# Performance work log

Measured on AMD Instinct MI355X. Metric: run time of the kernel, lower is better.

The kernel has to match this reference:

```python
import jax, jax.numpy as jnp
import numpy as np

N = 50000
E = 800000
IN_DIM = 256
HID_DIM = 256
OUT_DIM = 128


def _gcn(x, src, dst, W, b):
    # PyG GCNConv: h = W x; add self-loops; sym-normalized scatter-add; + bias
    h = x @ W  # [N, out]
    deg = jax.ops.segment_sum(jnp.ones_like(dst, dtype=h.dtype), dst, num_segments=N)
    dinv = jax.lax.rsqrt(jnp.maximum(deg, 1e-12))
    norm = dinv[src] * dinv[dst]  # [E+N]
    msg = h[src] * norm[:, None]  # gather + scale
    out = jax.ops.segment_sum(msg, dst, num_segments=N)  # scatter-add
    return out + b


def _with_self_loops(edge):
    loops = jnp.arange(N, dtype=edge.dtype)
    src = jnp.concatenate([edge[0], loops])
    dst = jnp.concatenate([edge[1], loops])
    return src, dst


def setup_inputs() -> dict:
    key = jax.random.key(0)
    ks = jax.random.split(key, 20)
    d = {}
    d['x'] = jax.random.normal(ks[0], (N, IN_DIM), dtype=jnp.float32)
    d['edge_ppi'] = jax.random.randint(ks[1], (2, E), 0, N, dtype=jnp.int32)
    d['edge_path'] = jax.random.randint(ks[2], (2, E), 0, N, dtype=jnp.int32)
    d['edge_go'] = jax.random.randint(ks[3], (2, E), 0, N, dtype=jnp.int32)
    i = 4
    for name in ['ppi', 'path', 'go']:
        s1 = 1.0 / np.sqrt(IN_DIM)
        s2 = 1.0 / np.sqrt(HID_DIM)
        d[f'{name}_w1'] = jax.random.uniform(ks[i], (IN_DIM, HID_DIM), jnp.float32, -s1, s1); i += 1
        d[f'{name}_b1'] = jnp.zeros((HID_DIM,), jnp.float32)
        d[f'{name}_w2'] = jax.random.uniform(ks[i], (HID_DIM, OUT_DIM), jnp.float32, -s2, s2); i += 1
        d[f'{name}_b2'] = jnp.zeros((OUT_DIM,), jnp.float32)
    sa = 1.0 / np.sqrt(OUT_DIM)
    d['attn_w'] = jax.random.uniform(ks[i], (OUT_DIM, 1), jnp.float32, -sa, sa)
    d['attn_b'] = jnp.zeros((1,), jnp.float32)
    return d


def reference(x, edge_ppi, edge_path, edge_go,
              ppi_w1, ppi_b1, ppi_w2, ppi_b2,
              path_w1, path_b1, path_w2, path_b2,
              go_w1, go_b1, go_w2, go_b2,
              attn_w, attn_b):
    feats = []
    for edge, w1, b1, w2, b2 in [
        (edge_ppi, ppi_w1, ppi_b1, ppi_w2, ppi_b2),
        (edge_path, path_w1, path_b1, path_w2, path_b2),
        (edge_go, go_w1, go_b1, go_w2, go_b2),
    ]:
        src, dst = _with_self_loops(edge)
        h = jax.nn.relu(_gcn(x, src, dst, w1, b1))
        feats.append(_gcn(h, src, dst, w2, b2))
    all_feat = jnp.stack(feats, axis=1)  # [N, 3, out]
    attn = jax.nn.softmax(all_feat @ attn_w + attn_b, axis=1)  # [N, 3, 1]
    return jnp.sum(all_feat * attn, axis=1)  # [N, out]
```

## Files before the change

kernel.cpp:

```cpp
#include <hip/hip_runtime.h>

#define NN 50000
#define NE 800000
#define BINS 98
#define CAP 12288
#define EPB 4096
#define P1B ((NE + EPB - 1) / EPB)
#define BINB (3 * P1B)
#define WB ((NN + 3) / 4)

typedef __attribute__((ext_vector_type(8))) short short8;
typedef __attribute__((ext_vector_type(4))) float f32x4;
typedef __attribute__((ext_vector_type(8))) unsigned short ushort8v;
typedef __attribute__((ext_vector_type(4))) unsigned short ushort4v;
typedef _Float16 half8 __attribute__((ext_vector_type(8)));

__device__ __forceinline__ ushort f2h(float f) {
    _Float16 h = (_Float16)f;
    return __builtin_bit_cast(ushort, h);
}
__device__ __forceinline__ float h2f(ushort u) {
    return (float)__builtin_bit_cast(_Float16, u);
}

__device__ __forceinline__ int wave_incl_scan(int v, int lane) {
#pragma unroll
    for (int d = 1; d < 64; d <<= 1) {
        int u = __shfl_up(v, d);
        if (lane >= d) v += u;
    }
    return v;
}


__global__ __launch_bounds__(256) void k_setup(
    const int* __restrict__ e0, const int* __restrict__ e1,
    const int* __restrict__ e2, int* __restrict__ g_cur,
    unsigned* __restrict__ g_bins,
    const float* __restrict__ x, ushort* __restrict__ x16,
    const float* __restrict__ w1a, const float* __restrict__ w1b,
    const float* __restrict__ w1c, ushort* __restrict__ BT1all,
    const float* __restrict__ w2a, const float* __restrict__ w2b,
    const float* __restrict__ w2c, ushort* __restrict__ BT2all) {
    const int tid = threadIdx.x;

    if (blockIdx.x < BINB) {
        const int br = blockIdx.x / P1B;
        const int cb = blockIdx.x % P1B;
        const int* ep = (br == 0 ? e0 : br == 1 ? e1 : e2);
        const int e_base = cb * EPB;

        __shared__ int s_cnt[BINS];
        __shared__ int s_start[BINS];
        __shared__ int s_cur[BINS];
        __shared__ int s_gb[BINS];
        __shared__ unsigned s_stage[EPB];

        if (tid < BINS) s_cnt[tid] = 0;
        __syncthreads();

        int4 s4[4], d4[4];
        bool valid[4];
#pragma unroll
        for (int i = 0; i < 4; ++i) {
            int idx = e_base + i * 1024 + tid * 4;
            valid[i] = (idx < NE);
            if (valid[i]) {
                s4[i] = *(const int4*)&ep[idx];
                d4[i] = *(const int4*)&ep[NE + idx];
                atomicAdd(&s_cnt[d4[i].x >> 9], 1);
                atomicAdd(&s_cnt[d4[i].y >> 9], 1);
                atomicAdd(&s_cnt[d4[i].z >> 9], 1);
                atomicAdd(&s_cnt[d4[i].w >> 9], 1);
            }
        }
        __syncthreads();
        if (tid == 0) {
            int run = 0;
            for (int b = 0; b < BINS; ++b) {
                s_start[b] = run;
                run += s_cnt[b];
            }
        }
        __syncthreads();
        if (tid < BINS) {
            s_cur[tid] = s_start[tid];
            int c = s_cnt[tid];
            int pc = (c + 15) & ~15;
            s_gb[tid] = (c > 0) ? atomicAdd(&g_cur[br * BINS + tid], pc) : 0;
        }
        __syncthreads();

#pragma unroll
        for (int i = 0; i < 4; ++i) {
            if (valid[i]) {
                int ss[4] = {s4[i].x, s4[i].y, s4[i].z, s4[i].w};
                int dd[4] = {d4[i].x, d4[i].y, d4[i].z, d4[i].w};
#pragma unroll
                for (int q = 0; q < 4; ++q) {
                    int bin = dd[q] >> 9;
                    int pos = atomicAdd(&s_cur[bin], 1);
                    s_stage[pos] = ((unsigned)(dd[q] & 511) << 16) | (unsigned)ss[q];
                }
            }
        }
        __syncthreads();

        for (int b = 0; b < BINS; ++b) {
            int c = s_cnt[b];
            if (c == 0) continue;
            int st = s_start[b];
            int gb = s_gb[b];
            int pc = (c + 15) & ~15;
            if (gb + pc > CAP) pc = (gb < CAP) ? (CAP - gb) : 0;
            size_t obase = (size_t)(br * BINS + b) * CAP + gb;
            for (int j = tid; j < pc; j += 256)
                g_bins[obase + j] = (j < c) ? s_stage[st + j] : 0x80000000u;
        }
        return;
    }

    int bb = blockIdx.x - BINB;
    if (bb < WB) {
        const int wid = tid >> 6, lane = tid & 63;
        const int row = bb * 4 + wid;
        if (row >= NN) return;
        float4 v = *(const float4*)&x[(size_t)row * 256 + lane * 4];
        ushort4 o;
        o.x = f2h(v.x); o.y = f2h(v.y); o.z = f2h(v.z); o.w = f2h(v.w);
        *(ushort4*)&x16[(size_t)row * 256 + lane * 4] = o;
        return;
    }
    bb -= WB;
    if (bb < 768) {
        int idx = bb * 256 + tid;
        int b = idx >> 16, r = idx & 65535;
        int k = r >> 8, n = r & 255;
        const float* W = (b == 0 ? w1a : b == 1 ? w1b : w1c);
        BT1all[(size_t)b * 65536 + (size_t)n * 256 + k] = f2h(W[r]);
        return;
    }
    bb -= 768;
    {
        int idx = bb * 256 + tid;
        int b = idx >> 15, r = idx & 32767;
        int k = r >> 7, n = r & 127;
        const float* W = (b == 0 ? w2a : b == 1 ? w2b : w2c);
        BT2all[(size_t)b * 32768 + (size_t)n * 256 + k] = f2h(W[r]);
    }
}


#define BGB 391

__global__ __launch_bounds__(512) void k_build_gemm1(
    const unsigned* __restrict__ g_bins, const int* __restrict__ g_cur,
    ushort* __restrict__ g_csr, int* __restrict__ seg3, int* __restrict__ cnt3,
    float* __restrict__ dinv3,
    const ushort* __restrict__ x16, const ushort* __restrict__ BT1all,
    ushort* __restrict__ hs16all) {
    __shared__ ushort sA[2][128 * 32];
    __shared__ ushort sB[2][256 * 32];
    __shared__ int s_cnt[512];
    __shared__ int s_wsum[8];

    const int t = threadIdx.x, lane = t & 63, wid = t >> 6;

    if (blockIdx.x < 3 * BINS) {
        const int bid = blockIdx.x;
        const int br = bid / BINS;
        const int b2 = bid % BINS;
        const size_t base = (size_t)bid * CAP;
        const int node0 = b2 << 9;

        s_cnt[t] = 0;
        __syncthreads();

        const int total = min(g_cur[bid], CAP);
        for (int j = t; j < total; j += 512) {
            unsigned p = g_bins[base + j];
            if (!(p & 0x80000000u)) atomicAdd(&s_cnt[(p >> 16) & 0x1FF], 1);
        }
        __syncthreads();

        int c = s_cnt[t];
        int incl = wave_incl_scan(c, lane);
        if (lane == 63) s_wsum[wid] = incl;
        __syncthreads();
        int wpre = 0;
        for (int i = 0; i < wid; ++i) wpre += s_wsum[i];
        int ex = wpre + incl - c;

        int node = node0 + t;
        if (node < NN) {
            int g = br * NN + node;
            seg3[g] = (int)base + ex;
            cnt3[g] = c;
            dinv3[g] = rsqrtf((float)(c + 1));
        }
        __syncthreads();
        s_cnt[t] = ex;
        __syncthreads();

        for (int j = t; j < total; j += 512) {
            unsigned p = g_bins[base + j];
            if (!(p & 0x80000000u)) {
                int loc = (p >> 16) & 0x1FF;
                int pos = atomicAdd(&s_cnt[loc], 1);
                g_csr[base + pos] = (ushort)(p & 0xFFFFu);
            }
        }
        return;
    }

    constexpr int BM = 128, BN = 256, N = 256, KK = 256, BK = 32;
    constexpr int NW = 8, WGN = 4, NSTEP = KK / BK;
    const int sbid = blockIdx.x - 3 * BINS;
    int q = sbid >> 3, r = sbid & 7;
    int bid = (q / 3) * 8 + r;
    int kb = q % 3;
    if (bid >= BGB) return;

    const ushort* BT = BT1all + (size_t)kb * 65536;
    ushort* C = hs16all + (size_t)kb * NN * 256;
    const int wm = (wid / WGN) * 64, wn = (wid % WGN) * 64;
    const int bm = bid * BM;

    f32x4 zero = {0.f, 0.f, 0.f, 0.f};
    f32x4 acc[4][4];
#pragma unroll
    for (int m = 0; m < 4; ++m)
#pragma unroll
        for (int n = 0; n < 4; ++n) acc[m][n] = zero;

    auto stage = [&](int buf, int kt) {
        {
            int off = wid << 10;
            int la = off + lane * 16;
            int row = la >> 6;
            int slot = (la >> 4) & 3;
            int scol = (slot ^ (row & 3)) << 4;
            int grow = bm + row;
            if (grow > NN - 1) grow = NN - 1;
            const char* ga = (const char*)x16 + (size_t)grow * (KK * 2) + kt * 2 + scol;
            __builtin_amdgcn_global_load_lds(
                (__attribute__((address_space(1))) const void*)ga,
                (__attribute__((address_space(3))) void*)((char*)sA[buf] + off), 16, 0, 0);
        }
#pragma unroll
        for (int i = 0; i < 2; ++i) {
            int off = (wid + i * NW) << 10;
            int la = off + lane * 16;
            int row = la >> 6;
            int slot = (la >> 4) & 3;
            int scol = (slot ^ (row & 3)) << 4;
            const char* ga = (const char*)BT + (size_t)row * (KK * 2) + kt * 2 + scol;
            __builtin_amdgcn_global_load_lds(
                (__attribute__((address_space(1))) const void*)ga,
                (__attribute__((address_space(3))) void*)((char*)sB[buf] + off), 16, 0, 0);
        }
    };

    stage(0, 0);
    __syncthreads();

    int cur = 0;
    for (int ts = 0; ts < NSTEP; ++ts) {
        if (ts + 1 < NSTEP) stage(cur ^ 1, (ts + 1) * BK);

        const int s = lane >> 4;
        const int r0 = lane & 15;
        short8 af[4], bf[4];
#pragma unroll
        for (int m = 0; m < 4; ++m) {
            int row = wm + m * 16 + r0;
            af[m] = *(const short8*)((const char*)sA[cur] + row * 64 + ((s ^ (row & 3)) << 4));
        }
#pragma unroll
        for (int n = 0; n < 4; ++n) {
            int row = wn + n * 16 + r0;
            bf[n] = *(const short8*)((const char*)sB[cur] + row * 64 + ((s ^ (row & 3)) << 4));
        }
#pragma unroll
        for (int m = 0; m < 4; ++m)
#pragma unroll
            for (int n = 0; n < 4; ++n)
                acc[m][n] = __builtin_amdgcn_mfma_f32_16x16x32_f16(
                    __builtin_bit_cast(half8, af[m]), __builtin_bit_cast(half8, bf[n]),
                    acc[m][n], 0, 0, 0);
        __syncthreads();
        cur ^= 1;
    }

    const int cr0 = (lane >> 4) * 4;
    const int cc = lane & 15;
#pragma unroll
    for (int m = 0; m < 4; ++m) {
#pragma unroll
        for (int rg = 0; rg < 4; ++rg) {
            int row = bm + wm + m * 16 + cr0 + rg;
            if (row < NN) {
#pragma unroll
                for (int n = 0; n < 4; ++n)
                    C[(size_t)row * N + wn + n * 16 + cc] = f2h(acc[m][n][rg]);
            }
        }
    }
}


__global__ __launch_bounds__(256) void k_gemm2(
    const ushort* __restrict__ h1all, const ushort* __restrict__ BT2all,
    const float* __restrict__ dinv3, ushort* __restrict__ hs2all) {
    constexpr int BM = 128, BN = 128, N = 128, KK = 256, BK = 32;
    constexpr int NW = 4, WGN = 2, NSTEP = KK / BK;
    constexpr int MT = (NN + BM - 1) / BM;
    __shared__ ushort sA[2][BM * 32];
    __shared__ ushort sB[2][BN * 32];
    const int kb = blockIdx.x / MT;
    const int bid = blockIdx.x % MT;
    const ushort* Ab = h1all + (size_t)kb * NN * 256;
    const ushort* BT = BT2all + (size_t)kb * 32768;
    const float* dinv = dinv3 + (size_t)kb * NN;
    ushort* C = hs2all + (size_t)kb * NN * 128;
    const int t = threadIdx.x, lane = t & 63, wid = t >> 6;
    const int wm = (wid / WGN) * 64, wn = (wid % WGN) * 64;
    const int bm = bid * BM;

    f32x4 zero = {0.f, 0.f, 0.f, 0.f};
    f32x4 acc[4][4];
#pragma unroll
    for (int m = 0; m < 4; ++m)
#pragma unroll
        for (int n = 0; n < 4; ++n) acc[m][n] = zero;

    auto stage = [&](int buf, int kt) {
#pragma unroll
        for (int i = 0; i < 2; ++i) {
            int off = (wid + i * NW) << 10;
            int la = off + lane * 16;
            int row = la >> 6;
            int slot = (la >> 4) & 3;
            int scol = (slot ^ (row & 3)) << 4;
            int grow = bm + row;
            if (grow > NN - 1) grow = NN - 1;
            const char* ga = (const char*)Ab + (size_t)grow * (KK * 2) + kt * 2 + scol;
            __builtin_amdgcn_global_load_lds(
                (__attribute__((address_space(1))) const void*)ga,
                (__attribute__((address_space(3))) void*)((char*)sA[buf] + off), 16, 0, 0);
        }
#pragma unroll
        for (int i = 0; i < 2; ++i) {
            int off = (wid + i * NW) << 10;
            int la = off + lane * 16;
            int row = la >> 6;
            int slot = (la >> 4) & 3;
            int scol = (slot ^ (row & 3)) << 4;
            const char* ga = (const char*)BT + (size_t)row * (KK * 2) + kt * 2 + scol;
            __builtin_amdgcn_global_load_lds(
                (__attribute__((address_space(1))) const void*)ga,
                (__attribute__((address_space(3))) void*)((char*)sB[buf] + off), 16, 0, 0);
        }
    };

    stage(0, 0);
    __syncthreads();

    int cur = 0;
    for (int ts = 0; ts < NSTEP; ++ts) {
        if (ts + 1 < NSTEP) stage(cur ^ 1, (ts + 1) * BK);

        const int s = lane >> 4;
        const int r0 = lane & 15;
        short8 af[4], bf[4];
#pragma unroll
        for (int m = 0; m < 4; ++m) {
            int row = wm + m * 16 + r0;
            af[m] = *(const short8*)((const char*)sA[cur] + row * 64 + ((s ^ (row & 3)) << 4));
        }
#pragma unroll
        for (int n = 0; n < 4; ++n) {
            int row = wn + n * 16 + r0;
            bf[n] = *(const short8*)((const char*)sB[cur] + row * 64 + ((s ^ (row & 3)) << 4));
        }
#pragma unroll
        for (int m = 0; m < 4; ++m)
#pragma unroll
            for (int n = 0; n < 4; ++n)
                acc[m][n] = __builtin_amdgcn_mfma_f32_16x16x32_f16(
                    __builtin_bit_cast(half8, af[m]), __builtin_bit_cast(half8, bf[n]),
                    acc[m][n], 0, 0, 0);
        __syncthreads();
        cur ^= 1;
    }

    const int cr0 = (lane >> 4) * 4;
    const int cc = lane & 15;
#pragma unroll
    for (int m = 0; m < 4; ++m) {
#pragma unroll
        for (int rg = 0; rg < 4; ++rg) {
            int row = bm + wm + m * 16 + cr0 + rg;
            if (row < NN) {
                float dv = dinv[row];
#pragma unroll
                for (int n = 0; n < 4; ++n)
                    C[(size_t)row * N + wn + n * 16 + cc] = f2h(acc[m][n][rg] * dv);
            }
        }
    }
}


#define UTOT (3 * 12500)

__global__ __launch_bounds__(256) void k_agg1(const ushort* __restrict__ hs16all,
                                              const int* __restrict__ seg3,
                                              const int* __restrict__ cnt3,
                                              const ushort* __restrict__ g_csr,
                                              const float* __restrict__ dinv3,
                                              const float* __restrict__ b1a,
                                              const float* __restrict__ b1b,
                                              const float* __restrict__ b1c,
                                              ushort* __restrict__ h1all) {
    const int x = blockIdx.x & 7, j = blockIdx.x >> 3;
    const int start = (x * UTOT) >> 3;
    const int end = ((x + 1) * UTOT) >> 3;
    const int u = start + j;
    if (u >= end) return;
    const int b = u / 12500;
    const int blk = u % 12500;

    const int wid = threadIdx.x >> 6;
    const int lane = threadIdx.x & 63;
    const int node = blk * 4 + wid;
    if (node >= NN) return;
    const int half = lane >> 5, l32 = lane & 31;
    const int g = b * NN + node;
    const ushort* hs = hs16all + (size_t)b * NN * 256;
    const float* dv = dinv3 + (size_t)b * NN;
    const ushort* csr = g_csr + seg3[g];
    const int len = cnt3[g] + 1;
    const size_t colb = (size_t)l32 * 8;

    float acc[8] = {0.f, 0.f, 0.f, 0.f, 0.f, 0.f, 0.f, 0.f};
    int i = half;
    for (; i + 6 < len; i += 8) {
        int s0 = (i == 0) ? node : (int)csr[i - 1];
        int s1 = (int)csr[i + 1];
        int s2 = (int)csr[i + 3];
        int s3 = (int)csr[i + 5];
        float d0 = dv[s0], d1 = dv[s1], d2 = dv[s2], d3 = dv[s3];
        ushort8v v0 = *(const ushort8v*)&hs[(size_t)s0 * 256 + colb];
        ushort8v v1 = *(const ushort8v*)&hs[(size_t)s1 * 256 + colb];
        ushort8v v2 = *(const ushort8v*)&hs[(size_t)s2 * 256 + colb];
        ushort8v v3 = *(const ushort8v*)&hs[(size_t)s3 * 256 + colb];
#pragma unroll
        for (int jq = 0; jq < 8; ++jq)
            acc[jq] += (d0 * h2f(v0[jq]) + d1 * h2f(v1[jq])) +
                       (d2 * h2f(v2[jq]) + d3 * h2f(v3[jq]));
    }
    for (; i < len; i += 2) {
        int s = (i == 0) ? node : (int)csr[i - 1];
        float d = dv[s];
        ushort8v v = *(const ushort8v*)&hs[(size_t)s * 256 + colb];
#pragma unroll
        for (int jq = 0; jq < 8; ++jq) acc[jq] += d * h2f(v[jq]);
    }
#pragma unroll
    for (int jq = 0; jq < 8; ++jq) acc[jq] += __shfl_xor(acc[jq], 32);

    if (half == 0) {
        const float* bias = (b == 0 ? b1a : b == 1 ? b1b : b1c);
        const float di = dv[node];
        ushort8v o;
#pragma unroll
        for (int jq = 0; jq < 8; ++jq) {
            float r = fmaxf(di * acc[jq] + bias[l32 * 8 + jq], 0.f);
            o[jq] = f2h(r);
        }
        *(ushort8v*)&h1all[((size_t)b * NN + node) * 256 + colb] = o;
    }
}


__global__ __launch_bounds__(256) void k_final(const ushort* __restrict__ hs2all,
                                               const int* __restrict__ seg3,
                                               const int* __restrict__ cnt3,
                                               const ushort* __restrict__ g_csr,
                                               const float* __restrict__ dinv3,
                                               const float* __restrict__ b2a,
                                               const float* __restrict__ b2b,
                                               const float* __restrict__ b2c,
                                               const float* __restrict__ attn_w,
                                               const float* __restrict__ attn_b,
                                               float* __restrict__ out) {
    const int wid = threadIdx.x >> 6;
    const int lane = threadIdx.x & 63;
    const int node = blockIdx.x * 4 + wid;
    if (node >= NN) return;
    const int half = lane >> 5, l32 = lane & 31;
    const size_t colb = (size_t)l32 * 4;

    float f[3][4];
#pragma unroll
    for (int b = 0; b < 3; ++b) {
        const int g = b * NN + node;
        const ushort* hs = hs2all + (size_t)b * NN * 128;
        const ushort* csr = g_csr + seg3[g];
        const int len = cnt3[g] + 1;
        float acc[4] = {0.f, 0.f, 0.f, 0.f};
        int i = half;
        for (; i + 6 < len; i += 8) {
            int s0 = (i == 0) ? node : (int)csr[i - 1];
            int s1 = (int)csr[i + 1];
            int s2 = (int)csr[i + 3];
            int s3 = (int)csr[i + 5];
            ushort4v v0 = *(const ushort4v*)&hs[(size_t)s0 * 128 + colb];
            ushort4v v1 = *(const ushort4v*)&hs[(size_t)s1 * 128 + colb];
            ushort4v v2 = *(const ushort4v*)&hs[(size_t)s2 * 128 + colb];
            ushort4v v3 = *(const ushort4v*)&hs[(size_t)s3 * 128 + colb];
#pragma unroll
            for (int j = 0; j < 4; ++j)
                acc[j] += (h2f(v0[j]) + h2f(v1[j])) + (h2f(v2[j]) + h2f(v3[j]));
        }
        for (; i < len; i += 2) {
            int s = (i == 0) ? node : (int)csr[i - 1];
            ushort4v v = *(const ushort4v*)&hs[(size_t)s * 128 + colb];
#pragma unroll
            for (int j = 0; j < 4; ++j) acc[j] += h2f(v[j]);
        }
#pragma unroll
        for (int j = 0; j < 4; ++j) acc[j] += __shfl_xor(acc[j], 32);
        const float* bias = (b == 0 ? b2a : b == 1 ? b2b : b2c);
        const float di = dinv3[g];
#pragma unroll
        for (int j = 0; j < 4; ++j) f[b][j] = di * acc[j] + bias[l32 * 4 + j];
    }

    float4 w = *(const float4*)&attn_w[l32 * 4];
    float s0 = f[0][0] * w.x + f[0][1] * w.y + f[0][2] * w.z + f[0][3] * w.w;
    float s1 = f[1][0] * w.x + f[1][1] * w.y + f[1][2] * w.z + f[1][3] * w.w;
    float s2 = f[2][0] * w.x + f[2][1] * w.y + f[2][2] * w.z + f[2][3] * w.w;
#pragma unroll
    for (int m = 16; m >= 1; m >>= 1) {
        s0 += __shfl_xor(s0, m);
        s1 += __shfl_xor(s1, m);
        s2 += __shfl_xor(s2, m);
    }
    float bb = attn_b[0];
    s0 += bb; s1 += bb; s2 += bb;
    float mx = fmaxf(s0, fmaxf(s1, s2));
    float e0 = expf(s0 - mx), e1 = expf(s1 - mx), e2 = expf(s2 - mx);
    float inv = 1.f / (e0 + e1 + e2);
    e0 *= inv; e1 *= inv; e2 *= inv;

    if (half == 0) {
        float4 o;
        o.x = f[0][0] * e0 + f[1][0] * e1 + f[2][0] * e2;
        o.y = f[0][1] * e0 + f[1][1] * e1 + f[2][1] * e2;
        o.z = f[0][2] * e0 + f[1][2] * e1 + f[2][2] * e2;
        o.w = f[0][3] * e0 + f[1][3] * e1 + f[2][3] * e2;
        *(float4*)&out[(size_t)node * 128 + colb] = o;
    }
}


extern "C" void kernel_launch(void* const* d_in, const int* in_sizes, int n_in,
                              void* d_out, int out_size, void* d_ws, size_t ws_size,
                              hipStream_t stream) {
    const float* x = (const float*)d_in[0];
    const int* e0 = (const int*)d_in[1];
    const int* e1 = (const int*)d_in[2];
    const int* e2 = (const int*)d_in[3];
    const float* attn_w = (const float*)d_in[16];
    const float* attn_b = (const float*)d_in[17];

    char* ws = (char*)d_ws;
    size_t off = 0;
    auto alloc = [&](size_t bytes) -> void* {
        void* p = ws + off;
        off += (bytes + 255) & ~(size_t)255;
        return p;
    };

    int* g_cur      = (int*)alloc(3 * BINS * 4);
    int* seg3       = (int*)alloc((size_t)3 * NN * 4);
    int* cnt3       = (int*)alloc((size_t)3 * NN * 4);
    float* dinv3    = (float*)alloc((size_t)3 * NN * 4);
    ushort* g_csr   = (ushort*)alloc((size_t)3 * BINS * CAP * 2);
    ushort* x16     = (ushort*)alloc((size_t)NN * 256 * 2);
    ushort* hs16all = (ushort*)alloc((size_t)3 * NN * 256 * 2);
    ushort* h1all   = (ushort*)alloc((size_t)3 * NN * 256 * 2);
    unsigned* g_bins = (unsigned*)h1all;
    ushort* hs2all  = (ushort*)alloc((size_t)3 * NN * 128 * 2);
    ushort* BT1all  = (ushort*)alloc((size_t)3 * 256 * 256 * 2);
    ushort* BT2all  = (ushort*)alloc((size_t)3 * 128 * 256 * 2);

    hipMemsetAsync(g_cur, 0, 3 * BINS * 4, stream);

    k_setup<<<BINB + WB + 768 + 384, 256, 0, stream>>>(
        e0, e1, e2, g_cur, g_bins, x, x16,
        (const float*)d_in[4], (const float*)d_in[8], (const float*)d_in[12], BT1all,
        (const float*)d_in[6], (const float*)d_in[10], (const float*)d_in[14], BT2all);

    k_build_gemm1<<<3 * BINS + 1176, 512, 0, stream>>>(
        g_bins, g_cur, g_csr, seg3, cnt3, dinv3, x16, BT1all, hs16all);

    k_agg1<<<8 * ((UTOT + 7) / 8), 256, 0, stream>>>(
        hs16all, seg3, cnt3, g_csr, dinv3,
        (const float*)d_in[5], (const float*)d_in[9], (const float*)d_in[13], h1all);

    k_gemm2<<<3 * 391, 256, 0, stream>>>(h1all, BT2all, dinv3, hs2all);

    k_final<<<WB, 256, 0, stream>>>(hs2all, seg3, cnt3, g_csr, dinv3,
                                    (const float*)d_in[7], (const float*)d_in[11],
                                    (const float*)d_in[15], attn_w, attn_b,
                                    (float*)d_out);
}
```

Measured before the change: 403.1 us.

## Fuse layer-1 aggregation with layer-2 GEMM via shared-memory tile

Merges the first-layer neighbor aggregation and the second-layer GEMM into one kernel. Each block aggregates 64 nodes into a swizzled LDS tile, then runs MFMA against W2 read straight from global memory. This drops the h1 round trip through HBM and one kernel launch. In exchange, g_bins now needs its own buffer, each block serializes 16 nodes per wave, there is less parallelism (2346 blocks of 64 nodes instead of 37500 blocks of 4 nodes), and B fragments are no longer staged through LDS.

```diff
diff --git a/kernel.cpp b/kernel.cpp
--- a/kernel.cpp
+++ b/kernel.cpp
@@ -213,7 +213,7 @@
         return;
     }
 
-    constexpr int BM = 128, BN = 256, N = 256, KK = 256, BK = 32;
+    constexpr int BM = 128, N = 256, KK = 256, BK = 32;
     constexpr int NW = 8, WGN = 4, NSTEP = KK / BK;
     const int sbid = blockIdx.x - 3 * BINS;
     int q = sbid >> 3, r = sbid & 7;
@@ -309,177 +309,113 @@
 }
 
 
-__global__ __launch_bounds__(256) void k_gemm2(
-    const ushort* __restrict__ h1all, const ushort* __restrict__ BT2all,
-    const float* __restrict__ dinv3, ushort* __restrict__ hs2all) {
-    constexpr int BM = 128, BN = 128, N = 128, KK = 256, BK = 32;
-    constexpr int NW = 4, WGN = 2, NSTEP = KK / BK;
-    constexpr int MT = (NN + BM - 1) / BM;
-    __shared__ ushort sA[2][BM * 32];
-    __shared__ ushort sB[2][BN * 32];
-    const int kb = blockIdx.x / MT;
-    const int bid = blockIdx.x % MT;
-    const ushort* Ab = h1all + (size_t)kb * NN * 256;
-    const ushort* BT = BT2all + (size_t)kb * 32768;
-    const float* dinv = dinv3 + (size_t)kb * NN;
-    ushort* C = hs2all + (size_t)kb * NN * 128;
+__global__ __launch_bounds__(256) void k_agg1g2(
+    const ushort* __restrict__ hs16all, const int* __restrict__ seg3,
+    const int* __restrict__ cnt3, const ushort* __restrict__ g_csr,
+    const float* __restrict__ dinv3,
+    const float* __restrict__ b1a, const float* __restrict__ b1b,
+    const float* __restrict__ b1c,
+    const ushort* __restrict__ BT2all, ushort* __restrict__ hs2all) {
+    constexpr int TPB = (NN + 63) / 64;
+    const int br = blockIdx.x / TPB;
+    const int blk = blockIdx.x % TPB;
+    const int node0 = blk * 64;
     const int t = threadIdx.x, lane = t & 63, wid = t >> 6;
-    const int wm = (wid / WGN) * 64, wn = (wid % WGN) * 64;
-    const int bm = bid * BM;
-
+    const int half = lane >> 5, l32 = lane & 31;
+
+    __shared__ ushort h1s[64 * 256];
+
+    const ushort* hs = hs16all + (size_t)br * NN * 256;
+    const float* dv = dinv3 + (size_t)br * NN;
+    const float* bias = (br == 0 ? b1a : br == 1 ? b1b : b1c);
+    const size_t colb = (size_t)l32 * 8;
+
+#pragma unroll 1
+    for (int q = 0; q < 16; ++q) {
+        const int r = wid * 16 + q;
+        const int node = node0 + r;
+        if (node < NN) {
+            const int g = br * NN + node;
+            const ushort* csr = g_csr + seg3[g];
+            const int len = cnt3[g] + 1;
+
+            float acc[8] = {0.f, 0.f, 0.f, 0.f, 0.f, 0.f, 0.f, 0.f};
+            int i = half;
+            for (; i + 6 < len; i += 8) {
+                int s0 = (i == 0) ? node : (int)csr[i - 1];
+                int s1 = (int)csr[i + 1];
+                int s2 = (int)csr[i + 3];
+                int s3 = (int)csr[i + 5];
+                float d0 = dv[s0], d1 = dv[s1], d2 = dv[s2], d3 = dv[s3];
+                ushort8v v0 = *(const ushort8v*)&hs[(size_t)s0 * 256 + colb];
+                ushort8v v1 = *(const ushort8v*)&hs[(size_t)s1 * 256 + colb];
+                ushort8v v2 = *(const ushort8v*)&hs[(size_t)s2 * 256 + colb];
+                ushort8v v3 = *(const ushort8v*)&hs[(size_t)s3 * 256 + colb];
+#pragma unroll
+                for (int j = 0; j < 8; ++j)
+                    acc[j] += (d0 * h2f(v0[j]) + d1 * h2f(v1[j])) +
+                              (d2 * h2f(v2[j]) + d3 * h2f(v3[j]));
+            }
+            for (; i < len; i += 2) {
+                int s = (i == 0) ? node : (int)csr[i - 1];
+                float d = dv[s];
+                ushort8v v = *(const ushort8v*)&hs[(size_t)s * 256 + colb];
+#pragma unroll
+                for (int j = 0; j < 8; ++j) acc[j] += d * h2f(v[j]);
+            }
+#pragma unroll
+            for (int j = 0; j < 8; ++j) acc[j] += __shfl_xor(acc[j], 32);
+
+            if (half == 0) {
+                const float di = dv[node];
+                ushort8v o;
+#pragma unroll
+                for (int j = 0; j < 8; ++j) {
+                    float rr = fmaxf(di * acc[j] + bias[l32 * 8 + j], 0.f);
+                    o[j] = f2h(rr);
+                }
+                *(ushort8v*)((char*)h1s + r * 512 + ((l32 ^ (r & 7)) << 4)) = o;
+            }
+        } else if (half == 0) {
+            ushort8v z = {0, 0, 0, 0, 0, 0, 0, 0};
+            *(ushort8v*)((char*)h1s + r * 512 + ((l32 ^ (r & 7)) << 4)) = z;
+        }
+    }
+    __syncthreads();
+
+    const ushort* BT2 = BT2all + (size_t)br * 32768;
+    const int r0 = lane & 15, s = lane >> 4;
     f32x4 zero = {0.f, 0.f, 0.f, 0.f};
-    f32x4 acc[4][4];
-#pragma unroll
-    for (int m = 0; m < 4; ++m)
-#pragma unroll
-        for (int n = 0; n < 4; ++n) acc[m][n] = zero;
-
-    auto stage = [&](int buf, int kt) {
-#pragma unroll
-        for (int i = 0; i < 2; ++i) {
-            int off = (wid + i * NW) << 10;
-            int la = off + lane * 16;
-            int row = la >> 6;
-            int slot = (la >> 4) & 3;
-            int scol = (slot ^ (row & 3)) << 4;
-            int grow = bm + row;
-            if (grow > NN - 1) grow = NN - 1;
-            const char* ga = (const char*)Ab + (size_t)grow * (KK * 2) + kt * 2 + scol;
-            __builtin_amdgcn_global_load_lds(
-                (__attribute__((address_space(1))) const void*)ga,
-                (__attribute__((address_space(3))) void*)((char*)sA[buf] + off), 16, 0, 0);
-        }
-#pragma unroll
-        for (int i = 0; i < 2; ++i) {
-            int off = (wid + i * NW) << 10;
-            int la = off + lane * 16;
-            int row = la >> 6;
-            int slot = (la >> 4) & 3;
-            int scol = (slot ^ (row & 3)) << 4;
-            const char* ga = (const char*)BT + (size_t)row * (KK * 2) + kt * 2 + scol;
-            __builtin_amdgcn_global_load_lds(
-                (__attribute__((address_space(1))) const void*)ga,
-                (__attribute__((address_space(3))) void*)((char*)sB[buf] + off), 16, 0, 0);
-        }
-    };
-
-    stage(0, 0);
-    __syncthreads();
-
-    int cur = 0;
-    for (int ts = 0; ts < NSTEP; ++ts) {
-        if (ts + 1 < NSTEP) stage(cur ^ 1, (ts + 1) * BK);
-
-        const int s = lane >> 4;
-        const int r0 = lane & 15;
-        short8 af[4], bf[4];
-#pragma unroll
-        for (int m = 0; m < 4; ++m) {
-            int row = wm + m * 16 + r0;
-            af[m] = *(const short8*)((const char*)sA[cur] + row * 64 + ((s ^ (row & 3)) << 4));
-        }
-#pragma unroll
-        for (int n = 0; n < 4; ++n) {
-            int row = wn + n * 16 + r0;
-            bf[n] = *(const short8*)((const char*)sB[cur] + row * 64 + ((s ^ (row & 3)) << 4));
-        }
-#pragma unroll
-        for (int m = 0; m < 4; ++m)
-#pragma unroll
-            for (int n = 0; n < 4; ++n)
-                acc[m][n] = __builtin_amdgcn_mfma_f32_16x16x32_f16(
-                    __builtin_bit_cast(half8, af[m]), __builtin_bit_cast(half8, bf[n]),
-                    acc[m][n], 0, 0, 0);
-        __syncthreads();
-        cur ^= 1;
-    }
-
+    f32x4 acc2[8];
+#pragma unroll
+    for (int n = 0; n < 8; ++n) acc2[n] = zero;
+    const int arow = wid * 16 + r0;
+#pragma unroll
+    for (int ks = 0; ks < 8; ++ks) {
+        const int kt = ks * 32;
+        const int slot = (ks * 4 + s) ^ (r0 & 7);
+        short8 a = *(const short8*)((const char*)h1s + arow * 512 + (slot << 4));
+#pragma unroll
+        for (int n = 0; n < 8; ++n) {
+            short8 bfr = *(const short8*)&BT2[(size_t)(n * 16 + r0) * 256 + kt + s * 8];
+            acc2[n] = __builtin_amdgcn_mfma_f32_16x16x32_f16(
+                __builtin_bit_cast(half8, a), __builtin_bit_cast(half8, bfr),
+                acc2[n], 0, 0, 0);
+        }
+    }
+
+    const int cc = lane & 15;
     const int cr0 = (lane >> 4) * 4;
-    const int cc = lane & 15;
-#pragma unroll
-    for (int m = 0; m < 4; ++m) {
-#pragma unroll
-        for (int rg = 0; rg < 4; ++rg) {
-            int row = bm + wm + m * 16 + cr0 + rg;
-            if (row < NN) {
-                float dv = dinv[row];
-#pragma unroll
-                for (int n = 0; n < 4; ++n)
-                    C[(size_t)row * N + wn + n * 16 + cc] = f2h(acc[m][n][rg] * dv);
-            }
-        }
-    }
-}
-
-
-#define UTOT (3 * 12500)
-
-__global__ __launch_bounds__(256) void k_agg1(const ushort* __restrict__ hs16all,
-                                              const int* __restrict__ seg3,
-                                              const int* __restrict__ cnt3,
-                                              const ushort* __restrict__ g_csr,
-                                              const float* __restrict__ dinv3,
-                                              const float* __restrict__ b1a,
-                                              const float* __restrict__ b1b,
-                                              const float* __restrict__ b1c,
-                                              ushort* __restrict__ h1all) {
-    const int x = blockIdx.x & 7, j = blockIdx.x >> 3;
-    const int start = (x * UTOT) >> 3;
-    const int end = ((x + 1) * UTOT) >> 3;
-    const int u = start + j;
-    if (u >= end) return;
-    const int b = u / 12500;
-    const int blk = u % 12500;
-
-    const int wid = threadIdx.x >> 6;
-    const int lane = threadIdx.x & 63;
-    const int node = blk * 4 + wid;
-    if (node >= NN) return;
-    const int half = lane >> 5, l32 = lane & 31;
-    const int g = b * NN + node;
-    const ushort* hs = hs16all + (size_t)b * NN * 256;
-    const float* dv = dinv3 + (size_t)b * NN;
-    const ushort* csr = g_csr + seg3[g];
-    const int len = cnt3[g] + 1;
-    const size_t colb = (size_t)l32 * 8;
-
-    float acc[8] = {0.f, 0.f, 0.f, 0.f, 0.f, 0.f, 0.f, 0.f};
-    int i = half;
-    for (; i + 6 < len; i += 8) {
-        int s0 = (i == 0) ? node : (int)csr[i - 1];
-        int s1 = (int)csr[i + 1];
-        int s2 = (int)csr[i + 3];
-        int s3 = (int)csr[i + 5];
-        float d0 = dv[s0], d1 = dv[s1], d2 = dv[s2], d3 = dv[s3];
-        ushort8v v0 = *(const ushort8v*)&hs[(size_t)s0 * 256 + colb];
-        ushort8v v1 = *(const ushort8v*)&hs[(size_t)s1 * 256 + colb];
-        ushort8v v2 = *(const ushort8v*)&hs[(size_t)s2 * 256 + colb];
-        ushort8v v3 = *(const ushort8v*)&hs[(size_t)s3 * 256 + colb];
-#pragma unroll
-        for (int jq = 0; jq < 8; ++jq)
-            acc[jq] += (d0 * h2f(v0[jq]) + d1 * h2f(v1[jq])) +
-                       (d2 * h2f(v2[jq]) + d3 * h2f(v3[jq]));
-    }
-    for (; i < len; i += 2) {
-        int s = (i == 0) ? node : (int)csr[i - 1];
-        float d = dv[s];
-        ushort8v v = *(const ushort8v*)&hs[(size_t)s * 256 + colb];
-#pragma unroll
-        for (int jq = 0; jq < 8; ++jq) acc[jq] += d * h2f(v[jq]);
-    }
-#pragma unroll
-    for (int jq = 0; jq < 8; ++jq) acc[jq] += __shfl_xor(acc[jq], 32);
-
-    if (half == 0) {
-        const float* bias = (b == 0 ? b1a : b == 1 ? b1b : b1c);
-        const float di = dv[node];
-        ushort8v o;
-#pragma unroll
-        for (int jq = 0; jq < 8; ++jq) {
-            float r = fmaxf(di * acc[jq] + bias[l32 * 8 + jq], 0.f);
-            o[jq] = f2h(r);
-        }
-        *(ushort8v*)&h1all[((size_t)b * NN + node) * 256 + colb] = o;
+#pragma unroll
+    for (int rg = 0; rg < 4; ++rg) {
+        const int node = node0 + wid * 16 + cr0 + rg;
+        if (node < NN) {
+            float dvv = dv[node];
+            ushort* orow = hs2all + ((size_t)br * NN + node) * 128;
+#pragma unroll
+            for (int n = 0; n < 8; ++n)
+                orow[n * 16 + cc] = f2h(acc2[n][rg] * dvv);
+        }
     }
 }
 
@@ -589,10 +525,9 @@
     int* cnt3       = (int*)alloc((size_t)3 * NN * 4);
     float* dinv3    = (float*)alloc((size_t)3 * NN * 4);
     ushort* g_csr   = (ushort*)alloc((size_t)3 * BINS * CAP * 2);
+    unsigned* g_bins = (unsigned*)alloc((size_t)3 * BINS * CAP * 4);
     ushort* x16     = (ushort*)alloc((size_t)NN * 256 * 2);
     ushort* hs16all = (ushort*)alloc((size_t)3 * NN * 256 * 2);
-    ushort* h1all   = (ushort*)alloc((size_t)3 * NN * 256 * 2);
-    unsigned* g_bins = (unsigned*)h1all;
     ushort* hs2all  = (ushort*)alloc((size_t)3 * NN * 128 * 2);
     ushort* BT1all  = (ushort*)alloc((size_t)3 * 256 * 256 * 2);
     ushort* BT2all  = (ushort*)alloc((size_t)3 * 128 * 256 * 2);
@@ -607,11 +542,10 @@
     k_build_gemm1<<<3 * BINS + 1176, 512, 0, stream>>>(
         g_bins, g_cur, g_csr, seg3, cnt3, dinv3, x16, BT1all, hs16all);
 
-    k_agg1<<<8 * ((UTOT + 7) / 8), 256, 0, stream>>>(
+    k_agg1g2<<<3 * ((NN + 63) / 64), 256, 0, stream>>>(
         hs16all, seg3, cnt3, g_csr, dinv3,
-        (const float*)d_in[5], (const float*)d_in[9], (const float*)d_in[13], h1all);
-
-    k_gemm2<<<3 * 391, 256, 0, stream>>>(h1all, BT2all, dinv3, hs2all);
+        (const float*)d_in[5], (const float*)d_in[9], (const float*)d_in[13],
+        BT2all, hs2all);
 
     k_final<<<WB, 256, 0, stream>>>(hs2all, seg3, cnt3, g_csr, dinv3,
                                     (const float*)d_in[7], (const float*)d_in[11],
```

After: 482.4 us. 1.2x slower.
